# Kernel optimization log

Measured on AMD Instinct MI355X. Metric: run time of the kernel, lower is better.

## Reference

```python
import jax, jax.numpy as jnp
import numpy as np

WS = 8        # window size
NH = 8        # num heads


def setup_inputs() -> dict:
    key = jax.random.key(0)
    ks = jax.random.split(key, 6)
    B, C, H, W = 8, 256, 64, 64
    Cr = C // 4
    s = lambda n: 1.0 / np.sqrt(n)
    return {
        "x": jax.random.normal(ks[0], (B, C, H, W), jnp.float32),
        "ca_w1": jax.random.normal(ks[1], (Cr, C), jnp.float32) * s(C),
        "ca_b1": jnp.zeros((Cr,), jnp.float32),
        "ca_w2": jax.random.normal(ks[2], (C, Cr), jnp.float32) * s(Cr),
        "ca_b2": jnp.zeros((C,), jnp.float32),
        "in_proj_w": jax.random.normal(ks[3], (3 * C, C), jnp.float32) * s(C),
        "in_proj_b": jnp.zeros((3 * C,), jnp.float32),
        "out_proj_w": jax.random.normal(ks[4], (C, C), jnp.float32) * s(C),
        "out_proj_b": jnp.zeros((C,), jnp.float32),
    }


def reference(x, ca_w1, ca_b1, ca_w2, ca_b2, in_proj_w, in_proj_b, out_proj_w, out_proj_b):
    B, C, H, W = x.shape
    # ---- channel SE gate: AdaptiveAvgPool2d(1) -> 1x1 conv == linear ----
    pooled = x.mean(axis=(2, 3))                                   # [B, C]
    h1 = jax.nn.relu(pooled @ ca_w1.T + ca_b1)                     # [B, C/4]
    ca = jax.nn.sigmoid(h1 @ ca_w2.T + ca_b2)                      # [B, C]
    x = x * ca[:, :, None, None]

    # ---- window partition (non-overlapping unfold) ----
    Hw, Ww = H // WS, W // WS
    nwin = Hw * Ww
    xw = x.reshape(B, C, Hw, WS, Ww, WS).transpose(0, 1, 2, 4, 3, 5)   # [B,C,Hw,Ww,ws,ws]
    # view(B,C,nwin,ws*ws).permute(2,0,3,1).reshape(nwin*B, ws*ws, C)
    xw = xw.reshape(B, C, nwin, WS * WS).transpose(2, 0, 3, 1).reshape(nwin * B, WS * WS, C)

    # ---- nn.MultiheadAttention with batch_first=False: (L, N, E) ----
    # L = nwin*B (sequence!), N = ws*ws (batch!), E = C  -- faithful to source quirk
    L, N, _ = xw.shape
    hd = C // NH
    qkv = xw @ in_proj_w.T + in_proj_b                             # [L, N, 3C]
    q, k, v = jnp.split(qkv, 3, axis=-1)
    to_heads = lambda t: t.reshape(L, N, NH, hd).transpose(1, 2, 0, 3)  # [N, NH, L, hd]
    q, k, v = to_heads(q), to_heads(k), to_heads(v)
    scale = 1.0 / jnp.sqrt(jnp.asarray(hd, x.dtype))
    attn = jax.nn.softmax(jnp.einsum("nhld,nhmd->nhlm", q * scale, k), axis=-1)
    o = jnp.einsum("nhlm,nhmd->nhld", attn, v)                     # [N, NH, L, hd]
    o = o.transpose(2, 0, 1, 3).reshape(L, N, C)
    o = o @ out_proj_w.T + out_proj_b                              # [L, N, C]

    # ---- reshape back; nearest interpolate H*W -> H*W is identity ----
    o = o.reshape(nwin, B, WS * WS, C).transpose(1, 3, 0, 2)       # [B, C, nwin, ws*ws]
    x_out = o.reshape(B, C, H, W)
    return x + x_out
```

## Files before the change

kernel.cpp:

```cpp
#include <hip/hip_runtime.h>
#include <hip/hip_bf16.h>
#include <math.h>


typedef unsigned short ushort_t;
typedef unsigned int uint_t;
typedef __attribute__((ext_vector_type(8))) short bf16x8;
typedef __attribute__((ext_vector_type(4))) float f32x4;

#define ALPHA 0.25503486f

__device__ __forceinline__ uint_t pk_rne(float a, float b) {
    __hip_bfloat16 ha = __float2bfloat16(a), hb = __float2bfloat16(b);
    ushort_t ua = *(ushort_t*)&ha, ub = *(ushort_t*)&hb;
    return (uint_t)ua | ((uint_t)ub << 16);
}

__device__ __forceinline__ uint_t pk2(float a, float b) {
    union { float f; uint_t u; } ua, ub; ua.f = a; ub.f = b;
    return __builtin_amdgcn_perm(ua.u, ub.u, 0x03020706u);
}

__device__ __forceinline__ void gl_lds16(const ushort_t* g, ushort_t* l) {
    __builtin_amdgcn_global_load_lds(
        (__attribute__((address_space(1))) unsigned int*)(g),
        (__attribute__((address_space(3))) unsigned int*)(l), 16, 0, 0);
}

__global__ __launch_bounds__(256) void k_pool(const float* __restrict__ x,
                                              float* __restrict__ pooled) {
    int bc = blockIdx.x;
    const float4* row4 = (const float4*)(x + (size_t)bc * 4096);
    float s = 0.f;
    for (int i = threadIdx.x; i < 1024; i += 256) {
        float4 v = row4[i];
        s += v.x + v.y + v.z + v.w;
    }
    __shared__ float red[256];
    red[threadIdx.x] = s;
    __syncthreads();
    for (int o = 128; o > 0; o >>= 1) {
        if (threadIdx.x < o) red[threadIdx.x] += red[threadIdx.x + o];
        __syncthreads();
    }
    if (threadIdx.x == 0) pooled[bc] = red[0] * (1.f / 4096.f);
}

__global__ __launch_bounds__(256) void k_se(const float* __restrict__ pooled,
                                            const float* __restrict__ w1,
                                            const float* __restrict__ b1,
                                            const float* __restrict__ w2,
                                            const float* __restrict__ b2,
                                            float* __restrict__ ca) {
    __shared__ float sp[2048];
    __shared__ float sh1[512];
    int t = threadIdx.x;
    for (int i = t; i < 2048; i += 256) sp[i] = pooled[i];
    __syncthreads();
    for (int o = t; o < 512; o += 256) {
        int b = o >> 6, m = o & 63;
        float s = b1[m];
        const float* wr = w1 + (size_t)m * 256;
        const float* pr = sp + b * 256;
        for (int c = 0; c < 256; c++) s += pr[c] * wr[c];
        sh1[o] = s > 0.f ? s : 0.f;
    }
    __syncthreads();
    for (int o = t; o < 2048; o += 256) {
        int b = o >> 8, m = o & 255;
        float s = b2[m];
        const float* wr = w2 + (size_t)m * 64;
        const float* hr = sh1 + b * 64;
        for (int c = 0; c < 64; c++) s += hr[c] * wr[c];
        ca[o] = 1.f / (1.f + __expf(-s));
    }
}

__global__ __launch_bounds__(256) void k_cvt(const float* __restrict__ src,
                                             ushort_t* __restrict__ dst, int n8,
                                             int scale_n8, float scale) {
    int i = blockIdx.x * 256 + threadIdx.x;
    if (i >= n8) return;
    float sc = (i < scale_n8) ? scale : 1.f;
    const float4* s = (const float4*)src + (size_t)i * 2;
    float4 a = s[0], b = s[1];
    uint4 u;
    u.x = pk_rne(a.x * sc, a.y * sc); u.y = pk_rne(a.z * sc, a.w * sc);
    u.z = pk_rne(b.x * sc, b.y * sc); u.w = pk_rne(b.z * sc, b.w * sc);
    *(uint4*)(dst + (size_t)i * 8) = u;
}

#define GPAD 524
__global__ __launch_bounds__(256) void k_gate(const float* __restrict__ x,
                                              const float* __restrict__ ca,
                                              ushort_t* __restrict__ Ab) {
    __shared__ __align__(16) ushort_t Ls[32 * GPAD];
    __shared__ float sca[32];
    int bx = blockIdx.x;
    int b = bx >> 6, hw = (bx >> 3) & 7, c0 = (bx & 7) * 32;
    int t = threadIdx.x;
    if (t < 32) sca[t] = ca[b * 256 + c0 + t];
    __syncthreads();
    const float4* xb = (const float4*)(x + ((size_t)(b * 256 + c0) * 64 + hw * 8) * 64);
#pragma unroll
    for (int i = 0; i < 16; i++) {
        int f = i * 256 + t;
        int ch = f >> 7, rem = f & 127, r = rem >> 4, w4 = rem & 15;
        float4 v = xb[(size_t)ch * 1024 + r * 16 + w4];
        float g = sca[ch];
        uint2 u;
        u.x = pk_rne(v.x * g, v.y * g);
        u.y = pk_rne(v.z * g, v.w * g);
        *(uint2*)&Ls[ch * GPAD + r * 64 + w4 * 4] = u;
    }
    __syncthreads();
#pragma unroll
    for (int i = 0; i < 8; i++) {
        int q = i * 256 + t;
        int rr = q >> 2, part = q & 3;
        int ww = rr >> 6, p = rr & 63;
        int px = (p >> 3) * 64 + ww * 8 + (p & 7);
        const ushort_t* ls = &Ls[part * 8 * GPAD + px];
        uint4 u;
        u.x = (uint_t)ls[0]        | ((uint_t)ls[GPAD] << 16);
        u.y = (uint_t)ls[2 * GPAD] | ((uint_t)ls[3 * GPAD] << 16);
        u.z = (uint_t)ls[4 * GPAD] | ((uint_t)ls[5 * GPAD] << 16);
        u.w = (uint_t)ls[6 * GPAD] | ((uint_t)ls[7 * GPAD] << 16);
        size_t m = (size_t)(((hw * 8 + ww) * 8 + b) * 64 + p);
        *(uint4*)(Ab + m * 256 + c0 + part * 8) = u;
    }
}

__global__ __launch_bounds__(256, 2) void k_gemm_qkv2(const ushort_t* __restrict__ A,
                                                      const ushort_t* __restrict__ Bw,
                                                      const float* __restrict__ bias,
                                                      ushort_t* __restrict__ Qb,
                                                      ushort_t* __restrict__ Kb,
                                                      ushort_t* __restrict__ Vb) {
    __shared__ __align__(16) ushort_t As[128 * 64];
    __shared__ __align__(16) ushort_t Bs[128 * 64];
    int tid = threadIdx.x;
    int lane = tid & 63, wave = tid >> 6;
    int wm = wave >> 1, wn = wave & 1;
    int col = lane & 15, quad = lane >> 4;
    int n0 = blockIdx.x * 128;
    int m0 = blockIdx.y * 128;
    int cbase = wave * 64 + lane;

    f32x4 acc[4][4];
#pragma unroll
    for (int i = 0; i < 4; i++)
#pragma unroll
        for (int j = 0; j < 4; j++) acc[i][j] = (f32x4){0.f, 0.f, 0.f, 0.f};

    for (int k0 = 0; k0 < 256; k0 += 64) {
#pragma unroll
        for (int q = 0; q < 4; q++) {
            int c = q * 256 + cbase;
            int row = c >> 3;
            int kp = (c & 7) ^ (row & 7);
            gl_lds16(A + (size_t)(m0 + row) * 256 + k0 + kp * 8,
                     &As[(q * 4 + wave) * 512]);
            gl_lds16(Bw + (size_t)(n0 + row) * 256 + k0 + kp * 8,
                     &Bs[(q * 4 + wave) * 512]);
        }
        __syncthreads();
#pragma unroll
        for (int kk = 0; kk < 2; kk++) {
            bf16x8 af[4], bfg[4];
#pragma unroll
            for (int i = 0; i < 4; i++) {
                int row = wm * 64 + i * 16 + col;
                af[i] = *(const bf16x8*)&As[row * 64 + ((kk * 4 + quad) ^ (row & 7)) * 8];
            }
#pragma unroll
            for (int j = 0; j < 4; j++) {
                int row = wn * 64 + j * 16 + col;
                bfg[j] = *(const bf16x8*)&Bs[row * 64 + ((kk * 4 + quad) ^ (row & 7)) * 8];
            }
#pragma unroll
            for (int i = 0; i < 4; i++)
#pragma unroll
                for (int j = 0; j < 4; j++)
                    acc[i][j] = __builtin_amdgcn_mfma_f32_16x16x32_bf16(bfg[j], af[i], acc[i][j], 0, 0, 0);
        }
        __syncthreads();
    }

    int sec = n0 >> 8;
    ushort_t* dst = (sec == 0) ? Qb : (sec == 1) ? Kb : Vb;
    float bsc = (sec == 0) ? ALPHA : 1.f;
    int nb = (n0 & 255) + wn * 64 + quad * 4;
#pragma unroll
    for (int j = 0; j < 4; j++) {
        float4 bv = *(const float4*)(bias + n0 + wn * 64 + j * 16 + quad * 4);
        bv.x *= bsc; bv.y *= bsc; bv.z *= bsc; bv.w *= bsc;
#pragma unroll
        for (int i = 0; i < 4; i++) {
            int m = m0 + wm * 64 + i * 16 + col;
            uint2 st;
            st.x = pk_rne(acc[i][j][0] + bv.x, acc[i][j][1] + bv.y);
            st.y = pk_rne(acc[i][j][2] + bv.z, acc[i][j][3] + bv.w);
            *(uint2*)(dst + (size_t)m * 256 + nb + j * 16) = st;
        }
    }
}

__global__ __launch_bounds__(512, 4) void k_attn(const ushort_t* __restrict__ Qb,
                                                 const ushort_t* __restrict__ Kb,
                                                 const ushort_t* __restrict__ Vb,
                                                 ushort_t* __restrict__ AO) {
    __shared__ __align__(16) ushort_t Ks[512 * 32];
    __shared__ __align__(16) ushort_t Vt[32 * 512];
    int p = blockIdx.x >> 3, h = blockIdx.x & 7;
    int tid = threadIdx.x;
    int lane = tid & 63, wave = tid >> 6;
    int col = lane & 15, quad = lane >> 4;

#pragma unroll
    for (int it = 0; it < 4; it++) {
        int u = it * 512 + tid;
        int key = u >> 2, oct = u & 3;
        size_t grow = ((size_t)(key * 64 + p)) * 256 + h * 32 + oct * 8;
        int ck = oct ^ ((key >> 3) & 3);
        *(bf16x8*)&Ks[key * 32 + ck * 8] = *(const bf16x8*)(Kb + grow);
    }
#pragma unroll
    for (int it = 0; it < 2; it++) {
        int u = it * 512 + tid;
        int kp = u >> 2, oct = u & 3;
        int k0 = kp * 2;
        size_t g0 = ((size_t)(k0 * 64 + p)) * 256 + h * 32 + oct * 8;
        bf16x8 v0 = *(const bf16x8*)(Vb + g0);
        bf16x8 v1 = *(const bf16x8*)(Vb + g0 + 16384);
        int kc = kp >> 2;
#pragma unroll
        for (int j = 0; j < 8; j++) {
            int vc = oct * 8 + j;
            int kcs = kc ^ (vc & 7) ^ ((vc >> 3) << 1);
            uint_t pkv = (uint_t)(ushort_t)v0[j] | ((uint_t)(ushort_t)v1[j] << 16);
            *(uint_t*)&Vt[vc * 512 + kcs * 8 + (k0 & 7)] = pkv;
        }
    }

    bf16x8 qfrag[4];
#pragma unroll
    for (int i = 0; i < 4; i++) {
        int qt = wave * 4 + i;
        qfrag[i] = *(const bf16x8*)(Qb + ((size_t)((qt * 16 + col) * 64 + p)) * 256 + h * 32 + quad * 8);
    }

    f32x4 O0[4], O1[4];
    float qsum[4];
#pragma unroll
    for (int i = 0; i < 4; i++) {
        O0[i] = (f32x4){0.f, 0.f, 0.f, 0.f};
        O1[i] = (f32x4){0.f, 0.f, 0.f, 0.f};
        qsum[i] = 0.f;
    }
    const f32x4 zero = {0.f, 0.f, 0.f, 0.f};
    int R = col >> 2, r4 = lane & 3;
    int krow0 = 8 * R + r4;
    int vc0 = col, vc1 = col + 16;
    int sw0 = (vc0 & 7) ^ ((vc0 >> 3) << 1);
    int sw1 = (vc1 & 7) ^ ((vc1 >> 3) << 1);

    __syncthreads();

    for (int c = 0; c < 512; c += 32) {
        int row0 = c + krow0;
        int row1 = row0 + 4;
        int ckq = quad ^ ((row0 >> 3) & 3);
        bf16x8 kf0 = *(const bf16x8*)&Ks[row0 * 32 + ckq * 8];
        bf16x8 kf1 = *(const bf16x8*)&Ks[row1 * 32 + ckq * 8];
        int kc = (c >> 3) + quad;
        bf16x8 vf0 = *(const bf16x8*)&Vt[vc0 * 512 + ((kc ^ sw0) * 8)];
        bf16x8 vf1 = *(const bf16x8*)&Vt[vc1 * 512 + ((kc ^ sw1) * 8)];
#pragma unroll
        for (int i = 0; i < 4; i++) {
            f32x4 s0 = __builtin_amdgcn_mfma_f32_16x16x32_bf16(kf0, qfrag[i], zero, 0, 0, 0);
            f32x4 s1 = __builtin_amdgcn_mfma_f32_16x16x32_bf16(kf1, qfrag[i], zero, 0, 0, 0);
            float p0[4], p1[4];
#pragma unroll
            for (int r = 0; r < 4; r++) {
                p0[r] = __builtin_amdgcn_exp2f(s0[r]);
                p1[r] = __builtin_amdgcn_exp2f(s1[r]);
            }
            qsum[i] += ((p0[0] + p0[1]) + (p0[2] + p0[3])) + ((p1[0] + p1[1]) + (p1[2] + p1[3]));
            union { uint_t u[4]; bf16x8 v; } pb;
            pb.u[0] = pk2(p0[0], p0[1]);
            pb.u[1] = pk2(p0[2], p0[3]);
            pb.u[2] = pk2(p1[0], p1[1]);
            pb.u[3] = pk2(p1[2], p1[3]);
            O0[i] = __builtin_amdgcn_mfma_f32_16x16x32_bf16(vf0, pb.v, O0[i], 0, 0, 0);
            O1[i] = __builtin_amdgcn_mfma_f32_16x16x32_bf16(vf1, pb.v, O1[i], 0, 0, 0);
        }
    }

#pragma unroll
    for (int i = 0; i < 4; i++) {
        float s = qsum[i];
        s += __shfl_xor(s, 16);
        s += __shfl_xor(s, 32);
        float inv = 1.f / s;
        int qt = wave * 4 + i;
        ushort_t* dst = AO + ((size_t)((qt * 16 + col) * 64 + p)) * 256 + h * 32;
        uint2 st0, st1;
        st0.x = pk_rne(O0[i][0] * inv, O0[i][1] * inv);
        st0.y = pk_rne(O0[i][2] * inv, O0[i][3] * inv);
        st1.x = pk_rne(O1[i][0] * inv, O1[i][1] * inv);
        st1.y = pk_rne(O1[i][2] * inv, O1[i][3] * inv);
        *(uint2*)(dst + quad * 4) = st0;
        *(uint2*)(dst + 16 + quad * 4) = st1;
    }
}

__global__ __launch_bounds__(256, 2) void k_gemm_out2(const ushort_t* __restrict__ A,
                                                      const ushort_t* __restrict__ Bw,
                                                      const float* __restrict__ bias,
                                                      const float* __restrict__ x,
                                                      const float* __restrict__ ca,
                                                      float* __restrict__ out) {
    __shared__ __align__(16) ushort_t As[128 * 64];
    __shared__ __align__(16) ushort_t Bs[128 * 64];
    int tid = threadIdx.x;
    int lane = tid & 63, wave = tid >> 6;
    int wm = wave >> 1, wn = wave & 1;
    int col = lane & 15, quad = lane >> 4;
    int n0 = blockIdx.x * 128;
    int m0 = blockIdx.y * 128;
    int cbase = wave * 64 + lane;

    f32x4 acc[4][4];
#pragma unroll
    for (int i = 0; i < 4; i++)
#pragma unroll
        for (int j = 0; j < 4; j++) acc[i][j] = (f32x4){0.f, 0.f, 0.f, 0.f};

    for (int k0 = 0; k0 < 256; k0 += 64) {
#pragma unroll
        for (int q = 0; q < 4; q++) {
            int c = q * 256 + cbase;
            int row = c >> 3;
            int kp = (c & 7) ^ (row & 7);
            gl_lds16(A + (size_t)(m0 + row) * 256 + k0 + kp * 8,
                     &As[(q * 4 + wave) * 512]);
            gl_lds16(Bw + (size_t)(n0 + row) * 256 + k0 + kp * 8,
                     &Bs[(q * 4 + wave) * 512]);
        }
        __syncthreads();
#pragma unroll
        for (int kk = 0; kk < 2; kk++) {
            bf16x8 af[4], bfg[4];
#pragma unroll
            for (int i = 0; i < 4; i++) {
                int row = wm * 64 + i * 16 + col;
                af[i] = *(const bf16x8*)&As[row * 64 + ((kk * 4 + quad) ^ (row & 7)) * 8];
            }
#pragma unroll
            for (int j = 0; j < 4; j++) {
                int row = wn * 64 + j * 16 + col;
                bfg[j] = *(const bf16x8*)&Bs[row * 64 + ((kk * 4 + quad) ^ (row & 7)) * 8];
            }
#pragma unroll
            for (int i = 0; i < 4; i++)
#pragma unroll
                for (int j = 0; j < 4; j++)
                    acc[i][j] = __builtin_amdgcn_mfma_f32_16x16x32_bf16(bfg[j], af[i], acc[i][j], 0, 0, 0);
        }
        __syncthreads();
    }

    int lw = (m0 + wm * 64) >> 6;
    int b = lw & 7, w_idx = lw >> 3;
#pragma unroll
    for (int j = 0; j < 4; j++) {
        int nbase = n0 + wn * 64 + j * 16 + quad * 4;
        float4 bv = *(const float4*)(bias + nbase);
        float4 cv = *(const float4*)(ca + b * 256 + nbase);
#pragma unroll
        for (int i = 0; i < 4; i++) {
            int p = i * 16 + col;
#pragma unroll
            for (int r = 0; r < 4; r++) {
                int n = nbase + r;
                float bias_r = (r == 0) ? bv.x : (r == 1) ? bv.y : (r == 2) ? bv.z : bv.w;
                float ca_r = (r == 0) ? cv.x : (r == 1) ? cv.y : (r == 2) ? cv.z : cv.w;
                size_t oi = (((size_t)b * 256 + n) * 64 + w_idx) * 64 + p;
                out[oi] = acc[i][j][r] + bias_r + x[oi] * ca_r;
            }
        }
    }
}

extern "C" void kernel_launch(void* const* d_in, const int* in_sizes, int n_in,
                              void* d_out, int out_size, void* d_ws, size_t ws_size,
                              hipStream_t stream) {
    const float* x     = (const float*)d_in[0];
    const float* ca_w1 = (const float*)d_in[1];
    const float* ca_b1 = (const float*)d_in[2];
    const float* ca_w2 = (const float*)d_in[3];
    const float* ca_b2 = (const float*)d_in[4];
    const float* ipw   = (const float*)d_in[5];
    const float* ipb   = (const float*)d_in[6];
    const float* opw   = (const float*)d_in[7];
    const float* opb   = (const float*)d_in[8];
    float* out = (float*)d_out;

    char* ws = (char*)d_ws;
    const size_t MB16 = 16777216ull;
    ushort_t* Qb = (ushort_t*)(ws + 0);
    ushort_t* Kb = (ushort_t*)(ws + MB16);
    ushort_t* Vb = (ushort_t*)(ws + 2 * MB16);
    float* pooled = (float*)(ws + 3 * MB16);
    float* ca     = (float*)(ws + 3 * MB16 + 8192);

    ushort_t* Ab  = (ushort_t*)d_out;
    ushort_t* Wqb = (ushort_t*)((char*)d_out + MB16);
    ushort_t* Wob = Vb;

    k_cvt<<<96, 256, 0, stream>>>(ipw, Wqb, 24576, 8192, ALPHA);
    k_pool<<<2048, 256, 0, stream>>>(x, pooled);
    k_se<<<1, 256, 0, stream>>>(pooled, ca_w1, ca_b1, ca_w2, ca_b2, ca);
    k_gate<<<512, 256, 0, stream>>>(x, ca, Ab);
    k_gemm_qkv2<<<dim3(6, 256), 256, 0, stream>>>(Ab, Wqb, ipb, Qb, Kb, Vb);
    k_attn<<<512, 512, 0, stream>>>(Qb, Kb, Vb, Qb );
    k_cvt<<<32, 256, 0, stream>>>(opw, Wob, 8192, 0, 1.f);
    k_gemm_out2<<<dim3(2, 256), 256, 0, stream>>>(Qb, Wob, opb, x, ca, out);
}
```

Before: 206.8 us.

## Double-buffer LDS tiles and remap GEMM blocks across XCDs

Both bf16 GEMM kernels (the QKV projection and the output projection) now keep two LDS buffers. The global-to-LDS loads for the next K slice are issued before the MFMA work on the current slice, so load latency can overlap compute. Per-thread source pointers are computed once, outside the K loop. The 2D grid becomes a 1D grid whose block id is remapped so that consecutive tiles land on the same XCD, which should improve L2 reuse of the A rows. LDS use per block doubles to 64KB, which may limit occupancy if more than two blocks would otherwise fit.

```diff
diff --git a/kernel.cpp b/kernel.cpp
--- a/kernel.cpp
+++ b/kernel.cpp
@@ -137,46 +137,67 @@
                                                       ushort_t* __restrict__ Qb,
                                                       ushort_t* __restrict__ Kb,
                                                       ushort_t* __restrict__ Vb) {
-    __shared__ __align__(16) ushort_t As[128 * 64];
-    __shared__ __align__(16) ushort_t Bs[128 * 64];
+    __shared__ __align__(16) ushort_t As[2][8192];
+    __shared__ __align__(16) ushort_t Bs[2][8192];
     int tid = threadIdx.x;
     int lane = tid & 63, wave = tid >> 6;
     int wm = wave >> 1, wn = wave & 1;
     int col = lane & 15, quad = lane >> 4;
-    int n0 = blockIdx.x * 128;
-    int m0 = blockIdx.y * 128;
+    int orig = blockIdx.x;
+    int wgid = (orig & 7) * 192 + (orig >> 3);
+    int n0 = (wgid % 6) * 128;
+    int m0 = (wgid / 6) * 128;
     int cbase = wave * 64 + lane;
 
+    const ushort_t* asrc[4];
+    const ushort_t* bsrc[4];
+#pragma unroll
+    for (int q = 0; q < 4; q++) {
+        int c = q * 256 + cbase;
+        int row = c >> 3;
+        int kp = (c & 7) ^ (row & 7);
+        asrc[q] = A + (size_t)(m0 + row) * 256 + kp * 8;
+        bsrc[q] = Bw + (size_t)(n0 + row) * 256 + kp * 8;
+    }
+
     f32x4 acc[4][4];
 #pragma unroll
     for (int i = 0; i < 4; i++)
 #pragma unroll
         for (int j = 0; j < 4; j++) acc[i][j] = (f32x4){0.f, 0.f, 0.f, 0.f};
 
-    for (int k0 = 0; k0 < 256; k0 += 64) {
-#pragma unroll
-        for (int q = 0; q < 4; q++) {
-            int c = q * 256 + cbase;
-            int row = c >> 3;
-            int kp = (c & 7) ^ (row & 7);
-            gl_lds16(A + (size_t)(m0 + row) * 256 + k0 + kp * 8,
-                     &As[(q * 4 + wave) * 512]);
-            gl_lds16(Bw + (size_t)(n0 + row) * 256 + k0 + kp * 8,
-                     &Bs[(q * 4 + wave) * 512]);
-        }
-        __syncthreads();
+#pragma unroll
+    for (int q = 0; q < 4; q++) {
+        gl_lds16(asrc[q], &As[0][(q * 4 + wave) * 512]);
+        gl_lds16(bsrc[q], &Bs[0][(q * 4 + wave) * 512]);
+    }
+    __syncthreads();
+
+#pragma unroll
+    for (int t = 0; t < 4; t++) {
+        if (t < 3) {
+            int k0 = (t + 1) * 64;
+            int nb = (t + 1) & 1;
+#pragma unroll
+            for (int q = 0; q < 4; q++) {
+                gl_lds16(asrc[q] + k0, &As[nb][(q * 4 + wave) * 512]);
+                gl_lds16(bsrc[q] + k0, &Bs[nb][(q * 4 + wave) * 512]);
+            }
+        }
+        const ushort_t* Ac = As[t & 1];
+        const ushort_t* Bc = Bs[t & 1];
 #pragma unroll
         for (int kk = 0; kk < 2; kk++) {
             bf16x8 af[4], bfg[4];
 #pragma unroll
             for (int i = 0; i < 4; i++) {
                 int row = wm * 64 + i * 16 + col;
-                af[i] = *(const bf16x8*)&As[row * 64 + ((kk * 4 + quad) ^ (row & 7)) * 8];
+                af[i] = *(const bf16x8*)&Ac[row * 64 + ((kk * 4 + quad) ^ (row & 7)) * 8];
             }
 #pragma unroll
             for (int j = 0; j < 4; j++) {
                 int row = wn * 64 + j * 16 + col;
-                bfg[j] = *(const bf16x8*)&Bs[row * 64 + ((kk * 4 + quad) ^ (row & 7)) * 8];
+                bfg[j] = *(const bf16x8*)&Bc[row * 64 + ((kk * 4 + quad) ^ (row & 7)) * 8];
             }
 #pragma unroll
             for (int i = 0; i < 4; i++)
@@ -321,46 +342,67 @@
                                                       const float* __restrict__ x,
                                                       const float* __restrict__ ca,
                                                       float* __restrict__ out) {
-    __shared__ __align__(16) ushort_t As[128 * 64];
-    __shared__ __align__(16) ushort_t Bs[128 * 64];
+    __shared__ __align__(16) ushort_t As[2][8192];
+    __shared__ __align__(16) ushort_t Bs[2][8192];
     int tid = threadIdx.x;
     int lane = tid & 63, wave = tid >> 6;
     int wm = wave >> 1, wn = wave & 1;
     int col = lane & 15, quad = lane >> 4;
-    int n0 = blockIdx.x * 128;
-    int m0 = blockIdx.y * 128;
+    int orig = blockIdx.x;
+    int wgid = (orig & 7) * 64 + (orig >> 3);
+    int n0 = (wgid & 1) * 128;
+    int m0 = (wgid >> 1) * 128;
     int cbase = wave * 64 + lane;
 
+    const ushort_t* asrc[4];
+    const ushort_t* bsrc[4];
+#pragma unroll
+    for (int q = 0; q < 4; q++) {
+        int c = q * 256 + cbase;
+        int row = c >> 3;
+        int kp = (c & 7) ^ (row & 7);
+        asrc[q] = A + (size_t)(m0 + row) * 256 + kp * 8;
+        bsrc[q] = Bw + (size_t)(n0 + row) * 256 + kp * 8;
+    }
+
     f32x4 acc[4][4];
 #pragma unroll
     for (int i = 0; i < 4; i++)
 #pragma unroll
         for (int j = 0; j < 4; j++) acc[i][j] = (f32x4){0.f, 0.f, 0.f, 0.f};
 
-    for (int k0 = 0; k0 < 256; k0 += 64) {
-#pragma unroll
-        for (int q = 0; q < 4; q++) {
-            int c = q * 256 + cbase;
-            int row = c >> 3;
-            int kp = (c & 7) ^ (row & 7);
-            gl_lds16(A + (size_t)(m0 + row) * 256 + k0 + kp * 8,
-                     &As[(q * 4 + wave) * 512]);
-            gl_lds16(Bw + (size_t)(n0 + row) * 256 + k0 + kp * 8,
-                     &Bs[(q * 4 + wave) * 512]);
-        }
-        __syncthreads();
+#pragma unroll
+    for (int q = 0; q < 4; q++) {
+        gl_lds16(asrc[q], &As[0][(q * 4 + wave) * 512]);
+        gl_lds16(bsrc[q], &Bs[0][(q * 4 + wave) * 512]);
+    }
+    __syncthreads();
+
+#pragma unroll
+    for (int t = 0; t < 4; t++) {
+        if (t < 3) {
+            int k0 = (t + 1) * 64;
+            int nb = (t + 1) & 1;
+#pragma unroll
+            for (int q = 0; q < 4; q++) {
+                gl_lds16(asrc[q] + k0, &As[nb][(q * 4 + wave) * 512]);
+                gl_lds16(bsrc[q] + k0, &Bs[nb][(q * 4 + wave) * 512]);
+            }
+        }
+        const ushort_t* Ac = As[t & 1];
+        const ushort_t* Bc = Bs[t & 1];
 #pragma unroll
         for (int kk = 0; kk < 2; kk++) {
             bf16x8 af[4], bfg[4];
 #pragma unroll
             for (int i = 0; i < 4; i++) {
                 int row = wm * 64 + i * 16 + col;
-                af[i] = *(const bf16x8*)&As[row * 64 + ((kk * 4 + quad) ^ (row & 7)) * 8];
+                af[i] = *(const bf16x8*)&Ac[row * 64 + ((kk * 4 + quad) ^ (row & 7)) * 8];
             }
 #pragma unroll
             for (int j = 0; j < 4; j++) {
                 int row = wn * 64 + j * 16 + col;
-                bfg[j] = *(const bf16x8*)&Bs[row * 64 + ((kk * 4 + quad) ^ (row & 7)) * 8];
+                bfg[j] = *(const bf16x8*)&Bc[row * 64 + ((kk * 4 + quad) ^ (row & 7)) * 8];
             }
 #pragma unroll
             for (int i = 0; i < 4; i++)
@@ -423,8 +465,8 @@
     k_pool<<<2048, 256, 0, stream>>>(x, pooled);
     k_se<<<1, 256, 0, stream>>>(pooled, ca_w1, ca_b1, ca_w2, ca_b2, ca);
     k_gate<<<512, 256, 0, stream>>>(x, ca, Ab);
-    k_gemm_qkv2<<<dim3(6, 256), 256, 0, stream>>>(Ab, Wqb, ipb, Qb, Kb, Vb);
+    k_gemm_qkv2<<<1536, 256, 0, stream>>>(Ab, Wqb, ipb, Qb, Kb, Vb);
     k_attn<<<512, 512, 0, stream>>>(Qb, Kb, Vb, Qb );
     k_cvt<<<32, 256, 0, stream>>>(opw, Wob, 8192, 0, 1.f);
-    k_gemm_out2<<<dim3(2, 256), 256, 0, stream>>>(Qb, Wob, opb, x, ca, out);
-}
+    k_gemm_out2<<<512, 256, 0, stream>>>(Qb, Wob, opb, x, ca, out);
+}
```

After: 208.5 us. About the same (+0.8%).
